# Optimization experiments

Measured on AMD Instinct MI355X. Metric: run time of the kernel, lower is better.

The kernel has to match this reference:

```python
import jax, jax.numpy as jnp
import numpy as np

# static config (matches init_kwargs / chosen grid)
T, H, W = 8, 32, 32          # video token grid
WT, WH, WW = 4, 8, 8         # swin window
HEADS, HD = 16, 128
DIM = HEADS * HD             # 2048
LT = 256                     # text length
EPS = 1e-6
NT, NH, NW_ = T // WT, H // WH, W // WW
NWIN = NT * NH * NW_
WLEN = WT * WH * WW


def rmsnorm(x, g):
    # x: [..., HD], g: [HD]
    var = jnp.mean(x * x, axis=-1, keepdims=True)
    return x * jax.lax.rsqrt(var + EPS) * g


def setup_inputs() -> dict:
    key = jax.random.key(0)
    ks = jax.random.split(key, 8)
    s = 0.02
    Lv = T * H * W
    return {
        'vid': jax.random.normal(ks[0], (Lv, DIM), jnp.float32),
        'txt': jax.random.normal(ks[1], (LT, DIM), jnp.float32),
        'Wqkv_v': jax.random.normal(ks[2], (DIM, 3 * DIM), jnp.float32) * s,
        'bqkv_v': jnp.zeros((3 * DIM,), jnp.float32),
        'Wqkv_t': jax.random.normal(ks[3], (DIM, 3 * DIM), jnp.float32) * s,
        'bqkv_t': jnp.zeros((3 * DIM,), jnp.float32),
        'Wo_v': jax.random.normal(ks[4], (DIM, DIM), jnp.float32) * s,
        'bo_v': jnp.zeros((DIM,), jnp.float32),
        'Wo_t': jax.random.normal(ks[5], (DIM, DIM), jnp.float32) * s,
        'bo_t': jnp.zeros((DIM,), jnp.float32),
        'gq_v': jnp.ones((HD,), jnp.float32),
        'gk_v': jnp.ones((HD,), jnp.float32),
        'gq_t': jnp.ones((HD,), jnp.float32),
        'gk_t': jnp.ones((HD,), jnp.float32),
    }


def _forward(vid, txt, Wqkv_v, bqkv_v, Wqkv_t, bqkv_t, Wo_v, bo_v, Wo_t, bo_t,
             gq_v, gk_v, gq_t, gk_t):
    # per-modality QKV projections
    vqkv = vid @ Wqkv_v + bqkv_v                      # [Lv, 3*DIM]
    tqkv = txt @ Wqkv_t + bqkv_t                      # [LT, 3*DIM]
    # swin window partition: [T,H,W,C] -> [nWin, WLEN, 3, h, d]
    x = vqkv.reshape(NT, WT, NH, WH, NW_, WW, 3 * DIM)
    x = x.transpose(0, 2, 4, 1, 3, 5, 6).reshape(NWIN, WLEN, 3, HEADS, HD)
    vq, vk, vv = x[:, :, 0], x[:, :, 1], x[:, :, 2]
    t = tqkv.reshape(LT, 3, HEADS, HD)
    tq, tk, tv = t[:, 0], t[:, 1], t[:, 2]
    # QK norm (per-head RMSNorm with affine)
    vq, vk = rmsnorm(vq, gq_v), rmsnorm(vk, gk_v)
    tq, tk = rmsnorm(tq, gq_t), rmsnorm(tk, gk_t)
    # concat full text to every window (repeat_concat_idx)
    bt = lambda a: jnp.broadcast_to(a[None], (NWIN,) + a.shape)
    q = jnp.concatenate([vq, bt(tq)], axis=1)          # [nWin, S, h, d]
    k = jnp.concatenate([vk, bt(tk)], axis=1)
    v = jnp.concatenate([vv, bt(tv)], axis=1)
    # attention within each window (flash-varlen equivalent, equal lengths)
    scale = 1.0 / np.sqrt(HD).astype(np.float32)
    scores = jnp.einsum('nqhd,nkhd->nhqk', q, k) * scale
    p = jax.nn.softmax(scores, axis=-1)
    o = jnp.einsum('nhqk,nkhd->nqhd', p, v)            # [nWin, S, h, d]
    vo = o[:, :WLEN].reshape(NWIN, WLEN, DIM)
    to = o[:, WLEN:].mean(axis=0).reshape(LT, DIM)     # un-repeat text: mean over windows
    # window reverse -> flat [Lv, DIM]
    vo = vo.reshape(NT, NH, NW_, WT, WH, WW, DIM)
    vo = vo.transpose(0, 3, 1, 4, 2, 5, 6).reshape(T * H * W, DIM)
    return (vo @ Wo_v + bo_v, to @ Wo_t + bo_t)


def reference(vid, txt, Wqkv_v, bqkv_v, Wqkv_t, bqkv_t, Wo_v, bo_v, Wo_t, bo_t,
              gq_v, gk_v, gq_t, gk_t):
    return _forward(vid, txt, Wqkv_v, bqkv_v, Wqkv_t, bqkv_t, Wo_v, bo_v,
                    Wo_t, bo_t, gq_v, gk_v, gq_t, gk_t)
```

## Files before the change

### kernel.cpp

```cpp
#include <hip/hip_runtime.h>

typedef unsigned short u16;
typedef unsigned int   u32;
typedef __attribute__((ext_vector_type(8))) short short8;
typedef __attribute__((ext_vector_type(4))) float f32x4;

__device__ __forceinline__ u16 f2bf(float f) {
  union { float f; u32 u; } v; v.f = f;
  u32 r = v.u + 0x7fffu + ((v.u >> 16) & 1u);
  return (u16)(r >> 16);
}
__device__ __forceinline__ float bf2f(u32 bits) {
  union { u32 u; float f; } v; v.u = bits << 16; return v.f;
}
__device__ __forceinline__ void gl_lds16(const u16* g, u16* l) {
  __builtin_amdgcn_global_load_lds(
      (const __attribute__((address_space(1))) void*)g,
      (__attribute__((address_space(3))) void*)l, 16, 0, 0);
}

static constexpr int DIM  = 2048;
static constexpr int NQKV = 6144;

__global__ __launch_bounds__(256) void conv_f32_bf16(const float* __restrict__ in,
                                                     u16* __restrict__ out, int n4) {
  int id = blockIdx.x * 256 + threadIdx.x;
  if (id >= n4) return;
  float4 v = ((const float4*)in)[id];
  u32 lo = (u32)f2bf(v.x) | ((u32)f2bf(v.y) << 16);
  u32 hi = (u32)f2bf(v.z) | ((u32)f2bf(v.w) << 16);
  ((uint2*)out)[id] = make_uint2(lo, hi);
}

__global__ void tconv_kernel(const float* __restrict__ W, u16* __restrict__ Wt, int K, int N) {
  __shared__ float t[32][33];
  int tx = threadIdx.x, ty = threadIdx.y;
  int n0 = blockIdx.x * 32, k0 = blockIdx.y * 32;
  #pragma unroll
  for (int i = 0; i < 4; ++i)
    t[ty + i*8][tx] = W[(size_t)(k0 + ty + i*8) * N + n0 + tx];
  __syncthreads();
  #pragma unroll
  for (int i = 0; i < 4; ++i)
    Wt[(size_t)(n0 + ty + i*8) * K + k0 + tx] = f2bf(t[tx][ty + i*8]);
}

__global__ __launch_bounds__(256) void rms_kernel(u16* __restrict__ x,
                                                  const float* __restrict__ g, int nrows) {
  int w = threadIdx.x >> 6, lane = threadIdx.x & 63;
  int rid = blockIdx.x * 4 + w;
  if (rid >= nrows) return;
  u32* row = (u32*)x + (size_t)rid * 64;
  u32 u = row[lane];
  float f0 = bf2f(u & 0xffffu), f1 = bf2f(u >> 16);
  float s = f0*f0 + f1*f1;
  #pragma unroll
  for (int off = 1; off <= 32; off <<= 1) s += __shfl_xor(s, off);
  float r = rsqrtf(s * (1.0f/128.0f) + 1e-6f);
  float g0 = g[lane*2], g1 = g[lane*2+1];
  row[lane] = (u32)f2bf(f0*r*g0) | ((u32)f2bf(f1*r*g1) << 16);
}

template<int EPI>
__global__ __launch_bounds__(512, 2)
void gemm256(const u16* __restrict__ A, const u16* __restrict__ Bt,
             const float* __restrict__ bias,
             u16* __restrict__ o0, u16* __restrict__ o1, u16* __restrict__ o2,
             float* __restrict__ of, int ldo, int M, int N, int K)
{
  __shared__ __align__(16) u16 As[4][256*32];
  __shared__ __align__(16) u16 Bs[4][256*32];
  const int NT = K >> 5;
  int tid = threadIdx.x, lane = tid & 63, w = tid >> 6;
  int l15 = lane & 15, l4 = lane >> 4;
  int wm = w >> 2, wn = w & 3;

  int nbx = gridDim.x;
  int nwg = nbx * gridDim.y;
  int bid = blockIdx.y * nbx + blockIdx.x;
  int cpx = nwg >> 3;
  int swz = (bid & 7) * cpx + (bid >> 3);
  int n0 = (swz % nbx) * 256, m0 = (swz / nbx) * 256;

  int srow = tid >> 2, skc = tid & 3;
  const u16* aS = A  + (size_t)(m0 + srow) * K + skc * 8;
  const u16* bS = Bt + (size_t)(n0 + srow) * K + skc * 8;
  const size_t halfStride = 128 * (size_t)K;
  const int ldsBase = w * 512;

  #define STAGE_A(slot, tt, half) \
    gl_lds16(aS + (size_t)(tt)*32 + (half)*halfStride, &As[slot][(half)*4096 + ldsBase])
  #define STAGE_B(slot, tt, half) \
    gl_lds16(bS + (size_t)(tt)*32 + (half)*halfStride, &Bs[slot][(half)*4096 + ldsBase])

  #pragma unroll
  for (int pt = 0; pt < 3; ++pt) {
    STAGE_A(pt, pt, 0); STAGE_A(pt, pt, 1);
    STAGE_B(pt, pt, 0); STAGE_B(pt, pt, 1);
  }

  f32x4 acc[8][4] = {};

  for (int t = 0; t < NT; ++t) {
    if (t < NT - 2)       asm volatile("s_waitcnt vmcnt(8)" ::: "memory");
    else if (t == NT - 2) asm volatile("s_waitcnt vmcnt(4)" ::: "memory");
    else                  asm volatile("s_waitcnt vmcnt(0)" ::: "memory");
    __builtin_amdgcn_s_barrier();
    asm volatile("" ::: "memory");

    const u16* ab = As[t & 3];
    const u16* bb = Bs[t & 3];
    bool st = (t + 3 < NT);
    int slot = (t + 3) & 3;

    short8 bf_[4];
    #pragma unroll
    for (int j = 0; j < 4; ++j)
      bf_[j] = *(const short8*)(bb + (wn*64 + j*16 + l15)*32 + l4*8);

    short8 af[4];
    #pragma unroll
    for (int i = 0; i < 4; ++i)
      af[i] = *(const short8*)(ab + (wm*128 + i*16 + l15)*32 + l4*8);
    if (st) { STAGE_A(slot, t+3, 0); STAGE_A(slot, t+3, 1); }
    __builtin_amdgcn_s_setprio(1);
    #pragma unroll
    for (int i = 0; i < 4; ++i)
      #pragma unroll
      for (int j = 0; j < 4; ++j)
        acc[i][j] = __builtin_amdgcn_mfma_f32_16x16x32_bf16(af[i], bf_[j], acc[i][j], 0, 0, 0);
    __builtin_amdgcn_s_setprio(0);

    #pragma unroll
    for (int i = 0; i < 4; ++i)
      af[i] = *(const short8*)(ab + (wm*128 + 64 + i*16 + l15)*32 + l4*8);
    if (st) { STAGE_B(slot, t+3, 0); STAGE_B(slot, t+3, 1); }
    __builtin_amdgcn_s_setprio(1);
    #pragma unroll
    for (int i = 0; i < 4; ++i)
      #pragma unroll
      for (int j = 0; j < 4; ++j)
        acc[4+i][j] = __builtin_amdgcn_mfma_f32_16x16x32_bf16(af[i], bf_[j], acc[4+i][j], 0, 0, 0);
    __builtin_amdgcn_s_setprio(0);
  }
  #undef STAGE_A
  #undef STAGE_B

  #pragma unroll
  for (int i = 0; i < 8; ++i)
    #pragma unroll
    for (int j = 0; j < 4; ++j)
      #pragma unroll
      for (int r = 0; r < 4; ++r) {
        int m = m0 + wm*128 + i*16 + l4*4 + r;
        int n = n0 + wn*64  + j*16 + l15;
        float v = acc[i][j][r] + bias[n];
        if (EPI == 0) {
          int which = n >> 11, head = (n >> 7) & 15, d = n & 127;
          int t = m >> 10, hh = (m >> 5) & 31, ww = m & 31;
          int win = ((t>>2)<<4) + ((hh>>3)<<2) + (ww>>3);
          int p   = ((t&3)<<6) + ((hh&7)<<3) + (ww&7);
          u16* dst = which == 0 ? o0 : (which == 1 ? o1 : o2);
          dst[((size_t)(win*16 + head)*256 + p)*128 + d] = f2bf(v);
        } else {
          of[(size_t)m * ldo + n] = v;
        }
      }
}

template<int EPI>
__global__ __launch_bounds__(256)
void gemm128(const u16* __restrict__ A, const u16* __restrict__ Bt,
             const float* __restrict__ bias,
             u16* __restrict__ o0, u16* __restrict__ o1, u16* __restrict__ o2,
             float* __restrict__ of, int ldo, int M, int N, int K)
{
  __shared__ __align__(16) u16 As[128*32];
  __shared__ __align__(16) u16 Bs[128*32];
  int tid = threadIdx.x, lane = tid & 63, w = tid >> 6;
  int l15 = lane & 15, l4 = lane >> 4;
  int m0 = blockIdx.y * 128, n0 = blockIdx.x * 128;
  int wr = (w >> 1) * 64, wc = (w & 1) * 64;
  f32x4 acc[4][4] = {};

  int o0b = (w    )*1024 + lane*16;
  int o1b = (w + 4)*1024 + lane*16;
  int r0 = o0b >> 6, c0 = ((o0b >> 4) & 3) ^ ((r0 >> 1) & 3);
  int r1 = o1b >> 6, c1 = ((o1b >> 4) & 3) ^ ((r1 >> 1) & 3);
  const u16* a0 = A  + (size_t)(m0 + r0)*K + c0*8;
  const u16* a1 = A  + (size_t)(m0 + r1)*K + c1*8;
  const u16* b0 = Bt + (size_t)(n0 + r0)*K + c0*8;
  const u16* b1 = Bt + (size_t)(n0 + r1)*K + c1*8;
  u16* dA0 = As + (w    )*512;
  u16* dA1 = As + (w + 4)*512;
  u16* dB0 = Bs + (w    )*512;
  u16* dB1 = Bs + (w + 4)*512;

  for (int k0 = 0; k0 < K; k0 += 32) {
    gl_lds16(a0 + k0, dA0);
    gl_lds16(a1 + k0, dA1);
    gl_lds16(b0 + k0, dB0);
    gl_lds16(b1 + k0, dB1);
    __syncthreads();
    short8 af[4], bfr[4];
    #pragma unroll
    for (int t = 0; t < 4; ++t) {
      int ra = wr + t*16 + l15;
      af[t]  = *(const short8*)((const char*)As + ra*64 + ((l4 ^ ((ra>>1)&3))*16));
      int rb = wc + t*16 + l15;
      bfr[t] = *(const short8*)((const char*)Bs + rb*64 + ((l4 ^ ((rb>>1)&3))*16));
    }
    #pragma unroll
    for (int i = 0; i < 4; ++i)
      #pragma unroll
      for (int j = 0; j < 4; ++j)
        acc[i][j] = __builtin_amdgcn_mfma_f32_16x16x32_bf16(af[i], bfr[j], acc[i][j], 0, 0, 0);
    __syncthreads();
  }

  #pragma unroll
  for (int i = 0; i < 4; ++i)
    #pragma unroll
    for (int j = 0; j < 4; ++j)
      #pragma unroll
      for (int r = 0; r < 4; ++r) {
        int m = m0 + wr + i*16 + l4*4 + r;
        int n = n0 + wc + j*16 + l15;
        float v = acc[i][j][r] + bias[n];
        if (EPI == 1) {
          int which = n >> 11, head = (n >> 7) & 15, d = n & 127;
          u16* dst = which == 0 ? o0 : (which == 1 ? o1 : o2);
          dst[((size_t)head*256 + m)*128 + d] = f2bf(v);
        } else {
          of[(size_t)m * ldo + n] = v;
        }
      }
}

__global__ __launch_bounds__(512)
void attn_kernel(const u16* __restrict__ vq, const u16* __restrict__ vk, const u16* __restrict__ vv,
                 const u16* __restrict__ tq, const u16* __restrict__ tk, const u16* __restrict__ tv,
                 u16* __restrict__ vo, float* __restrict__ to_acc)
{
  __shared__ __align__(16) u16 Ks[64*128];
  __shared__ __align__(16) u16 Vts[128*64];
  __shared__ __align__(16) u16 Ps[8][16*72];
  int tid = threadIdx.x, lane = tid & 63, w = tid >> 6;
  int l15 = lane & 15, l4 = lane >> 4;
  int nh_ = blockIdx.x;
  int n = nh_ >> 4, h = nh_ & 15;
  int qt = blockIdx.y * 128 + w * 16;

  const u16* Qb = (qt < 256) ? (vq + ((size_t)nh_*256 + qt)*128)
                             : (tq + ((size_t)h  *256 + (qt-256))*128);
  short8 qf[4];
  #pragma unroll
  for (int dt = 0; dt < 4; ++dt)
    qf[dt] = *(const short8*)(Qb + l15*128 + l4*8 + dt*32);

  f32x4 o_[8] = {};
  float m_run[4] = {-1e30f,-1e30f,-1e30f,-1e30f};
  float l_run[4] = {0.f,0.f,0.f,0.f};
  const float scale = 0.08838834764831845f;

  for (int c = 0; c < 8; ++c) {
    int kb = c * 64;
    const u16* Kc = (kb < 256) ? (vk + ((size_t)nh_*256 + kb)*128)
                               : (tk + ((size_t)h  *256 + (kb-256))*128);
    const u16* Vc = (kb < 256) ? (vv + ((size_t)nh_*256 + kb)*128)
                               : (tv + ((size_t)h  *256 + (kb-256))*128);
    #pragma unroll
    for (int s = 0; s < 2; ++s) {
      int id = tid + s*512;
      int kr = id >> 4, c16 = id & 15;
      short8 kvv = *(const short8*)(Kc + kr*128 + c16*8);
      *(short8*)((char*)Ks + kr*256 + ((c16*16) ^ ((kr&7)<<4))) = kvv;
      short8 vvv = *(const short8*)(Vc + kr*128 + c16*8);
      #pragma unroll
      for (int j = 0; j < 8; ++j) {
        int d = c16*8 + j;
        int sw = ((d ^ (d>>3)) & 7) << 4;
        *(u16*)((char*)Vts + d*128 + ((kr*2) ^ sw)) = (u16)vvv[j];
      }
    }
    __syncthreads();

    f32x4 s4[4];
    #pragma unroll
    for (int kt = 0; kt < 4; ++kt) {
      f32x4 sa = {0.f,0.f,0.f,0.f};
      int key = kt*16 + l15;
      #pragma unroll
      for (int dt = 0; dt < 4; ++dt) {
        int c16b = l4 + dt*4;
        short8 kf = *(const short8*)((const char*)Ks + key*256 + ((c16b*16) ^ ((key&7)<<4)));
        sa = __builtin_amdgcn_mfma_f32_16x16x32_bf16(qf[dt], kf, sa, 0, 0, 0);
      }
      s4[kt] = sa;
    }

    float f_[4];
    #pragma unroll
    for (int r = 0; r < 4; ++r) {
      float mx = fmaxf(fmaxf(s4[0][r], s4[1][r]), fmaxf(s4[2][r], s4[3][r])) * scale;
      #pragma unroll
      for (int off = 1; off <= 8; off <<= 1) mx = fmaxf(mx, __shfl_xor(mx, off));
      float nm = fmaxf(m_run[r], mx);
      f_[r] = __expf(m_run[r] - nm);
      m_run[r] = nm;
    }
    float p[4][4];
    #pragma unroll
    for (int kt = 0; kt < 4; ++kt)
      #pragma unroll
      for (int r = 0; r < 4; ++r)
        p[kt][r] = __expf(s4[kt][r]*scale - m_run[r]);
    #pragma unroll
    for (int r = 0; r < 4; ++r) {
      float sum = p[0][r] + p[1][r] + p[2][r] + p[3][r];
      #pragma unroll
      for (int off = 1; off <= 8; off <<= 1) sum += __shfl_xor(sum, off);
      l_run[r] = l_run[r]*f_[r] + sum;
    }
    #pragma unroll
    for (int dt = 0; dt < 8; ++dt) {
      f32x4 t = o_[dt];
      t[0]*=f_[0]; t[1]*=f_[1]; t[2]*=f_[2]; t[3]*=f_[3];
      o_[dt] = t;
    }

    u16* pb = Ps[w];
    #pragma unroll
    for (int kt = 0; kt < 4; ++kt)
      #pragma unroll
      for (int r = 0; r < 4; ++r)
        pb[(l4*4 + r)*72 + kt*16 + l15] = f2bf(p[kt][r]);
    __syncthreads();
    #pragma unroll
    for (int ks = 0; ks < 2; ++ks) {
      short8 pa = *(const short8*)((const char*)pb + l15*144 + l4*16 + ks*64);
      #pragma unroll
      for (int dt = 0; dt < 8; ++dt) {
        int d = dt*16 + l15;
        int sw = ((d ^ (d>>3)) & 7) << 4;
        short8 vf = *(const short8*)((const char*)Vts + d*128 + ((l4*16 + ks*64) ^ sw));
        o_[dt] = __builtin_amdgcn_mfma_f32_16x16x32_bf16(pa, vf, o_[dt], 0, 0, 0);
      }
    }
    __syncthreads();
  }

  float inv[4];
  #pragma unroll
  for (int r = 0; r < 4; ++r) inv[r] = 1.0f / l_run[r];
  int nt = n >> 4, nh2 = (n >> 2) & 3, nw = n & 3;
  #pragma unroll
  for (int dt = 0; dt < 8; ++dt) {
    int d = dt*16 + l15;
    int col = h*128 + d;
    #pragma unroll
    for (int r = 0; r < 4; ++r) {
      float val = o_[dt][r] * inv[r];
      int q = qt + l4*4 + r;
      if (q < 256) {
        int wt = q >> 6, wh = (q >> 3) & 7, ww = q & 7;
        int rg = ((nt*4 + wt)*32 + (nh2*8 + wh))*32 + (nw*8 + ww);
        vo[(size_t)rg*2048 + col] = f2bf(val);
      } else {
        atomicAdd(to_acc + (size_t)(q - 256)*2048 + col, val * (1.0f/32.0f));
      }
    }
  }
}

extern "C" void kernel_launch(void* const* d_in, const int* in_sizes, int n_in,
                              void* d_out, int out_size, void* d_ws, size_t ws_size,
                              hipStream_t stream) {
  const float* vid    = (const float*)d_in[0];
  const float* txt    = (const float*)d_in[1];
  const float* Wqkv_v = (const float*)d_in[2];
  const float* bqkv_v = (const float*)d_in[3];
  const float* Wqkv_t = (const float*)d_in[4];
  const float* bqkv_t = (const float*)d_in[5];
  const float* Wo_v   = (const float*)d_in[6];
  const float* bo_v   = (const float*)d_in[7];
  const float* Wo_t   = (const float*)d_in[8];
  const float* bo_t   = (const float*)d_in[9];
  const float* gq_v   = (const float*)d_in[10];
  const float* gk_v   = (const float*)d_in[11];
  const float* gq_t   = (const float*)d_in[12];
  const float* gk_t   = (const float*)d_in[13];
  float* out = (float*)d_out;

  char* p = (char*)d_ws;
  u16* vid_bf   = (u16*)p;  p += 8192ull*2048*2;
  u16* txt_bf   = (u16*)p;  p += 256ull*2048*2;
  u16* Wqkv_v_t = (u16*)p;  p += 6144ull*2048*2;
  u16* Wqkv_t_t = (u16*)p;  p += 6144ull*2048*2;
  u16* Wo_v_t   = (u16*)p;  p += 2048ull*2048*2;
  u16* Wo_t_t   = (u16*)p;  p += 2048ull*2048*2;
  u16* vq_w     = (u16*)p;  p += 32ull*16*256*128*2;
  u16* vk_w     = (u16*)p;  p += 32ull*16*256*128*2;
  u16* vv_w     = (u16*)p;  p += 32ull*16*256*128*2;
  u16* tq_w     = (u16*)p;  p += 16ull*256*128*2;
  u16* tk_w     = (u16*)p;  p += 16ull*256*128*2;
  u16* tv_w     = (u16*)p;  p += 16ull*256*128*2;
  u16* vo_pre   = (u16*)p;  p += 8192ull*2048*2;
  float* to_pre = (float*)p; p += 256ull*2048*4;
  u16* to_bf    = (u16*)p;  p += 256ull*2048*2;

  hipMemsetAsync(to_pre, 0, 256ull*2048*4, stream);

  conv_f32_bf16<<<dim3(16384), dim3(256), 0, stream>>>(vid, vid_bf, 8192*2048/4);
  conv_f32_bf16<<<dim3(512),   dim3(256), 0, stream>>>(txt, txt_bf, 256*2048/4);
  tconv_kernel<<<dim3(192,64), dim3(32,8), 0, stream>>>(Wqkv_v, Wqkv_v_t, 2048, 6144);
  tconv_kernel<<<dim3(192,64), dim3(32,8), 0, stream>>>(Wqkv_t, Wqkv_t_t, 2048, 6144);
  tconv_kernel<<<dim3(64,64),  dim3(32,8), 0, stream>>>(Wo_v,   Wo_v_t,   2048, 2048);
  tconv_kernel<<<dim3(64,64),  dim3(32,8), 0, stream>>>(Wo_t,   Wo_t_t,   2048, 2048);

  gemm256<0><<<dim3(24,32), dim3(512), 0, stream>>>(vid_bf, Wqkv_v_t, bqkv_v,
      vq_w, vk_w, vv_w, nullptr, 0, 8192, NQKV, DIM);
  gemm128<1><<<dim3(48,2),  dim3(256), 0, stream>>>(txt_bf, Wqkv_t_t, bqkv_t,
      tq_w, tk_w, tv_w, nullptr, 0, 256, NQKV, DIM);

  rms_kernel<<<dim3(32768), dim3(256), 0, stream>>>(vq_w, gq_v, 32*16*256);
  rms_kernel<<<dim3(32768), dim3(256), 0, stream>>>(vk_w, gk_v, 32*16*256);
  rms_kernel<<<dim3(1024),  dim3(256), 0, stream>>>(tq_w, gq_t, 16*256);
  rms_kernel<<<dim3(1024),  dim3(256), 0, stream>>>(tk_w, gk_t, 16*256);

  attn_kernel<<<dim3(512,4), dim3(512), 0, stream>>>(vq_w, vk_w, vv_w, tq_w, tk_w, tv_w,
                                                     vo_pre, to_pre);

  conv_f32_bf16<<<dim3(512), dim3(256), 0, stream>>>(to_pre, to_bf, 256*2048/4);

  gemm256<2><<<dim3(8,32), dim3(512), 0, stream>>>(vo_pre, Wo_v_t, bo_v,
      nullptr, nullptr, nullptr, out, 2048, 8192, 2048, 2048);
  gemm128<2><<<dim3(16,2), dim3(256), 0, stream>>>(to_bf, Wo_t_t, bo_t,
      nullptr, nullptr, nullptr, out + 16777216, 2048, 256, 2048, 2048);
}
```

Baseline: 724.9 us.

## Fuse Q RMSNorm into attention, store V transposed, load K/V via global_load_lds

The QKV GEMM epilogues now write V in a transposed [head, d, pos] layout, so the attention kernel no longer does a per-element scalar transpose into LDS. K and V tiles are loaded with direct global-to-LDS 16-byte loads, using a matching XOR swizzle. The query RMSNorm is folded into the attention kernel's Q fragment load, removing two separate normalization launches and their round trips through global memory. In exchange, the transposed V stores in the GEMM epilogue are strided and less coalesced, and the P buffer padding changes.

```diff
diff --git a/kernel.cpp b/kernel.cpp
--- a/kernel.cpp
+++ b/kernel.cpp
@@ -160,8 +160,12 @@
           int t = m >> 10, hh = (m >> 5) & 31, ww = m & 31;
           int win = ((t>>2)<<4) + ((hh>>3)<<2) + (ww>>3);
           int p   = ((t&3)<<6) + ((hh&7)<<3) + (ww&7);
-          u16* dst = which == 0 ? o0 : (which == 1 ? o1 : o2);
-          dst[((size_t)(win*16 + head)*256 + p)*128 + d] = f2bf(v);
+          if (which == 2) {
+            o2[((size_t)(win*16 + head)*128 + d)*256 + p] = f2bf(v);
+          } else {
+            u16* dst = which == 0 ? o0 : o1;
+            dst[((size_t)(win*16 + head)*256 + p)*128 + d] = f2bf(v);
+          }
         } else {
           of[(size_t)m * ldo + n] = v;
         }
@@ -229,8 +233,12 @@
         float v = acc[i][j][r] + bias[n];
         if (EPI == 1) {
           int which = n >> 11, head = (n >> 7) & 15, d = n & 127;
-          u16* dst = which == 0 ? o0 : (which == 1 ? o1 : o2);
-          dst[((size_t)head*256 + m)*128 + d] = f2bf(v);
+          if (which == 2) {
+            o2[((size_t)head*128 + d)*256 + m] = f2bf(v);
+          } else {
+            u16* dst = which == 0 ? o0 : o1;
+            dst[((size_t)head*256 + m)*128 + d] = f2bf(v);
+          }
         } else {
           of[(size_t)m * ldo + n] = v;
         }
@@ -240,23 +248,53 @@
 __global__ __launch_bounds__(512)
 void attn_kernel(const u16* __restrict__ vq, const u16* __restrict__ vk, const u16* __restrict__ vv,
                  const u16* __restrict__ tq, const u16* __restrict__ tk, const u16* __restrict__ tv,
+                 const float* __restrict__ gq_v, const float* __restrict__ gq_t,
                  u16* __restrict__ vo, float* __restrict__ to_acc)
 {
   __shared__ __align__(16) u16 Ks[64*128];
-  __shared__ __align__(16) u16 Vts[128*64];
-  __shared__ __align__(16) u16 Ps[8][16*72];
+  __shared__ __align__(16) u16 Vt[128*64];
+  __shared__ __align__(16) u16 Ps[8][16*80];
   int tid = threadIdx.x, lane = tid & 63, w = tid >> 6;
   int l15 = lane & 15, l4 = lane >> 4;
   int nh_ = blockIdx.x;
-  int n = nh_ >> 4, h = nh_ & 15;
+  int h = nh_ & 15;
+  int n = nh_ >> 4;
   int qt = blockIdx.y * 128 + w * 16;
 
-  const u16* Qb = (qt < 256) ? (vq + ((size_t)nh_*256 + qt)*128)
-                             : (tq + ((size_t)h  *256 + (qt-256))*128);
+  const u16* Qb; const float* gq;
+  if (qt < 256) { Qb = vq + ((size_t)nh_*256 + qt)*128; gq = gq_v; }
+  else          { Qb = tq + ((size_t)h  *256 + (qt-256))*128; gq = gq_t; }
   short8 qf[4];
-  #pragma unroll
-  for (int dt = 0; dt < 4; ++dt)
+  float qv[4][8];
+  float ss = 0.f;
+  #pragma unroll
+  for (int dt = 0; dt < 4; ++dt) {
     qf[dt] = *(const short8*)(Qb + l15*128 + l4*8 + dt*32);
+    #pragma unroll
+    for (int j = 0; j < 8; ++j) {
+      float f = bf2f((u16)qf[dt][j]);
+      qv[dt][j] = f; ss += f*f;
+    }
+  }
+  ss += __shfl_xor(ss, 16); ss += __shfl_xor(ss, 32);
+  float rr = rsqrtf(ss * (1.0f/128.0f) + 1e-6f);
+  #pragma unroll
+  for (int dt = 0; dt < 4; ++dt) {
+    float4 g0 = *(const float4*)(gq + l4*8 + dt*32);
+    float4 g1 = *(const float4*)(gq + l4*8 + dt*32 + 4);
+    qf[dt][0] = (short)f2bf(qv[dt][0]*rr*g0.x); qf[dt][1] = (short)f2bf(qv[dt][1]*rr*g0.y);
+    qf[dt][2] = (short)f2bf(qv[dt][2]*rr*g0.z); qf[dt][3] = (short)f2bf(qv[dt][3]*rr*g0.w);
+    qf[dt][4] = (short)f2bf(qv[dt][4]*rr*g1.x); qf[dt][5] = (short)f2bf(qv[dt][5]*rr*g1.y);
+    qf[dt][6] = (short)f2bf(qv[dt][6]*rr*g1.z); qf[dt][7] = (short)f2bf(qv[dt][7]*rr*g1.w);
+  }
+
+  int oK0 = w*1024 + lane*16, oK1 = oK0 + 8192;
+  int kr0 = oK0 >> 8, kc0 = ((oK0 >> 4) & 15) ^ (kr0 & 7);
+  int kr1 = oK1 >> 8, kc1 = ((oK1 >> 4) & 15) ^ (kr1 & 7);
+  int vd0 = oK0 >> 7, vc0 = ((oK0 >> 4) & 7) ^ (vd0 & 7);
+  int vd1 = oK1 >> 7, vc1 = ((oK1 >> 4) & 7) ^ (vd1 & 7);
+  u16* KD0 = Ks + (w*1024)/2;  u16* KD1 = Ks + (w*1024 + 8192)/2;
+  u16* VD0 = Vt + (w*1024)/2;  u16* VD1 = Vt + (w*1024 + 8192)/2;
 
   f32x4 o_[8] = {};
   float m_run[4] = {-1e30f,-1e30f,-1e30f,-1e30f};
@@ -265,24 +303,13 @@
 
   for (int c = 0; c < 8; ++c) {
     int kb = c * 64;
-    const u16* Kc = (kb < 256) ? (vk + ((size_t)nh_*256 + kb)*128)
-                               : (tk + ((size_t)h  *256 + (kb-256))*128);
-    const u16* Vc = (kb < 256) ? (vv + ((size_t)nh_*256 + kb)*128)
-                               : (tv + ((size_t)h  *256 + (kb-256))*128);
-    #pragma unroll
-    for (int s = 0; s < 2; ++s) {
-      int id = tid + s*512;
-      int kr = id >> 4, c16 = id & 15;
-      short8 kvv = *(const short8*)(Kc + kr*128 + c16*8);
-      *(short8*)((char*)Ks + kr*256 + ((c16*16) ^ ((kr&7)<<4))) = kvv;
-      short8 vvv = *(const short8*)(Vc + kr*128 + c16*8);
-      #pragma unroll
-      for (int j = 0; j < 8; ++j) {
-        int d = c16*8 + j;
-        int sw = ((d ^ (d>>3)) & 7) << 4;
-        *(u16*)((char*)Vts + d*128 + ((kr*2) ^ sw)) = (u16)vvv[j];
-      }
-    }
+    const u16* Kc; const u16* Vb; int vkb;
+    if (kb < 256) { Kc = vk + ((size_t)nh_*256 + kb)*128; Vb = vv + (size_t)nh_*128*256; vkb = kb; }
+    else          { Kc = tk + ((size_t)h  *256 + (kb-256))*128; Vb = tv + (size_t)h*128*256; vkb = kb - 256; }
+    gl_lds16(Kc + kr0*128 + kc0*8, KD0);
+    gl_lds16(Kc + kr1*128 + kc1*8, KD1);
+    gl_lds16(Vb + (size_t)vd0*256 + vkb + vc0*8, VD0);
+    gl_lds16(Vb + (size_t)vd1*256 + vkb + vc1*8, VD1);
     __syncthreads();
 
     f32x4 s4[4];
@@ -293,7 +320,7 @@
       #pragma unroll
       for (int dt = 0; dt < 4; ++dt) {
         int c16b = l4 + dt*4;
-        short8 kf = *(const short8*)((const char*)Ks + key*256 + ((c16b*16) ^ ((key&7)<<4)));
+        short8 kf = *(const short8*)((const char*)Ks + key*256 + (((c16b ^ (key&7)))*16));
         sa = __builtin_amdgcn_mfma_f32_16x16x32_bf16(qf[dt], kf, sa, 0, 0, 0);
       }
       s4[kt] = sa;
@@ -334,16 +361,15 @@
     for (int kt = 0; kt < 4; ++kt)
       #pragma unroll
       for (int r = 0; r < 4; ++r)
-        pb[(l4*4 + r)*72 + kt*16 + l15] = f2bf(p[kt][r]);
+        pb[(l4*4 + r)*80 + kt*16 + l15] = f2bf(p[kt][r]);
     __syncthreads();
     #pragma unroll
     for (int ks = 0; ks < 2; ++ks) {
-      short8 pa = *(const short8*)((const char*)pb + l15*144 + l4*16 + ks*64);
+      short8 pa = *(const short8*)((const char*)pb + l15*160 + ks*64 + l4*16);
       #pragma unroll
       for (int dt = 0; dt < 8; ++dt) {
         int d = dt*16 + l15;
-        int sw = ((d ^ (d>>3)) & 7) << 4;
-        short8 vf = *(const short8*)((const char*)Vts + d*128 + ((l4*16 + ks*64) ^ sw));
+        short8 vf = *(const short8*)((const char*)Vt + d*128 + (((ks*4 + l4) ^ (d&7))<<4));
         o_[dt] = __builtin_amdgcn_mfma_f32_16x16x32_bf16(pa, vf, o_[dt], 0, 0, 0);
       }
     }
@@ -423,13 +449,11 @@
   gemm128<1><<<dim3(48,2),  dim3(256), 0, stream>>>(txt_bf, Wqkv_t_t, bqkv_t,
       tq_w, tk_w, tv_w, nullptr, 0, 256, NQKV, DIM);
 
-  rms_kernel<<<dim3(32768), dim3(256), 0, stream>>>(vq_w, gq_v, 32*16*256);
   rms_kernel<<<dim3(32768), dim3(256), 0, stream>>>(vk_w, gk_v, 32*16*256);
-  rms_kernel<<<dim3(1024),  dim3(256), 0, stream>>>(tq_w, gq_t, 16*256);
   rms_kernel<<<dim3(1024),  dim3(256), 0, stream>>>(tk_w, gk_t, 16*256);
 
   attn_kernel<<<dim3(512,4), dim3(512), 0, stream>>>(vq_w, vk_w, vv_w, tq_w, tk_w, tv_w,
-                                                     vo_pre, to_pre);
+                                                     gq_v, gq_t, vo_pre, to_pre);
 
   conv_f32_bf16<<<dim3(512), dim3(256), 0, stream>>>(to_pre, to_bf, 256*2048/4);
 
```

New measurement: 697.2 us. 3.8% less time.
